# Performance work log

Hardware: AMD Instinct MI355X
Metric: run time of the kernel (lower is better)

The kernel has to match this reference:

```python
import jax, jax.numpy as jnp
import numpy as np

BLOCK_SIZE = 3
SOBEL_PAD = 1  # sobel_size // 2
BLOCK_PAD = BLOCK_SIZE // 2

_SOBEL_X = jnp.array([[-1.0, 0.0, 1.0], [-2.0, 0.0, 2.0], [-1.0, 0.0, 1.0]], dtype=jnp.float32)[None, None]
_SOBEL_Y = jnp.array([[-1.0, -2.0, -1.0], [0.0, 0.0, 0.0], [1.0, 2.0, 1.0]], dtype=jnp.float32)[None, None]
_SUM_K = jnp.ones((1, 1, BLOCK_SIZE, BLOCK_SIZE), dtype=jnp.float32)


def _pad_replicate(x, p):
    return jnp.pad(x, ((0, 0), (0, 0), (p, p), (p, p)), mode='edge')


def _conv(x, k):
    return jax.lax.conv_general_dilated(
        x, k, window_strides=(1, 1), padding='VALID',
        dimension_numbers=('NCHW', 'OIHW', 'NCHW'))


def setup_inputs() -> dict:
    key = jax.random.key(0)
    image = jax.random.uniform(key, (8, 1, 1080, 1920), dtype=jnp.float32) * 255.0
    return {"image": image}


def reference(image) -> jnp.ndarray:
    img = image.astype(jnp.float32)
    img_p = _pad_replicate(img, SOBEL_PAD)
    Ix = _conv(img_p, _SOBEL_X)
    Iy = _conv(img_p, _SOBEL_Y)
    Ixx = Ix * Ix
    Iyy = Iy * Iy
    Ixy = Ix * Iy
    sum_Ixx = _conv(_pad_replicate(Ixx, BLOCK_PAD), _SUM_K)
    sum_Iyy = _conv(_pad_replicate(Iyy, BLOCK_PAD), _SUM_K)
    sum_Ixy = _conv(_pad_replicate(Ixy, BLOCK_PAD), _SUM_K)
    half_trace = (sum_Ixx + sum_Iyy) * 0.5
    diff_half = (sum_Ixx - sum_Iyy) * 0.5
    sqrt_disc = jnp.sqrt(diff_half * diff_half + sum_Ixy * sum_Ixy + 1e-10)
    lambda_min = half_trace - sqrt_disc
    return jnp.clip(lambda_min, 0.0)
```

## Files before the change

### kernel.cpp

```cpp
#include <hip/hip_runtime.h>

typedef float v4f __attribute__((ext_vector_type(4)));

#define IMG_H 1080
#define IMG_W 1920
#define NBATCH 8
#define LSTRIP 9
#define BROWS (4*LSTRIP)
#define NK (LSTRIP+4)
#define PF 3
#define RS 4


__global__ __launch_bounds__(256, 2)
void shi_tomasi_kernel(const float* __restrict__ img, float* __restrict__ out) {
    const int cg    = threadIdx.x & 63;
    const int strip = threadIdx.x >> 6;
    const int bx    = blockIdx.x;
    const int base  = bx * 240;
    const int c0    = base + 4 * (cg - 2);
    const int clA   = min(max(c0 - 2, 0), IMG_W - 4);
    const int clB   = min(max(c0 + 2, 0), IMG_W - 4);
    const int s0    = blockIdx.y * BROWS + strip * LSTRIP;
    const float* g  = img + (size_t)blockIdx.z * (IMG_H * IMG_W);
    float* outb     = out + (size_t)blockIdx.z * (IMG_H * IMG_W);

    const bool eL     = (bx == 0) && (cg == 2);
    const bool eR     = (bx == 7) && (cg == 61);
    const bool doSt   = (cg >= 2) && (cg < 62);
    const bool topFix = (s0 == 0);
    const bool botFix = (s0 + LSTRIP == IMG_H);

    const float* lpA = g + clA;
    const float* lpB = g + clB;

    v4f za[RS], zb[RS];
    #pragma unroll
    for (int k = 0; k < PF; ++k) {
        int lr = max(0, min(IMG_H - 1, s0 - 2 + k));
        za[k] = *(const v4f*)(lpA + (size_t)lr * IMG_W);
        zb[k] = *(const v4f*)(lpB + (size_t)lr * IMG_W);
    }

    float cdR[3][6], hsR[3][6];
    float hxx[3][4], hyy[3][4], hxy[3][4];

    #pragma unroll
    for (int k = 0; k < NK; ++k) {
        if (k + PF < NK) {
            int lr = min(IMG_H - 1, s0 + k + (PF - 2));
            za[(k + PF) % RS] = *(const v4f*)(lpA + (size_t)lr * IMG_W);
            zb[(k + PF) % RS] = *(const v4f*)(lpB + (size_t)lr * IMG_W);
        }

        {
            const v4f A = za[k % RS];
            const v4f B = zb[k % RS];
            const float zm2 = A.x;
            const float zm1 = eL ? A.x : A.y;
            const float z0  = eL ? A.x : A.z;
            const float z1  = eL ? A.y : A.w;
            const float z2  = eR ? B.z : B.x;
            const float z3  = eR ? B.w : B.y;
            const float z4  = eR ? B.w : B.z;
            const float z5  = B.w;

            float* cdw = cdR[k % 3];
            float* hsw = hsR[k % 3];
            cdw[0] = z0 - zm2;
            cdw[1] = z1 - zm1;
            cdw[2] = z2 - z0;
            cdw[3] = z3 - z1;
            cdw[4] = z4 - z2;
            cdw[5] = z5 - z3;
            hsw[0] = fmaf(2.0f, zm1, zm2) + z0;
            hsw[1] = fmaf(2.0f, z0, zm1) + z1;
            hsw[2] = fmaf(2.0f, z1, z0) + z2;
            hsw[3] = fmaf(2.0f, z2, z1) + z3;
            hsw[4] = fmaf(2.0f, z3, z2) + z4;
            hsw[5] = fmaf(2.0f, z4, z3) + z5;
        }

        if (k >= 2) {
            const int rr = k - 2;
            const int sm = rr % 3, sz = (rr + 1) % 3, sp = (rr + 2) % 3;

            float Ix[6], Iy[6];
            #pragma unroll
            for (int p = 0; p < 6; ++p) {
                Ix[p] = fmaf(2.0f, cdR[sz][p], cdR[sm][p]) + cdR[sp][p];
                Iy[p] = hsR[sp][p] - hsR[sm][p];
            }
            if (eL) { Ix[0] = Ix[1]; Iy[0] = Iy[1]; }
            if (eR) { Ix[5] = Ix[4]; Iy[5] = Iy[4]; }

            float xx[6], yy[6], xy[6];
            #pragma unroll
            for (int p = 0; p < 6; ++p) {
                xx[p] = Ix[p] * Ix[p];
                yy[p] = Iy[p] * Iy[p];
                xy[p] = Ix[p] * Iy[p];
            }
            {
                float* hx = hxx[rr % 3];
                float* hy = hyy[rr % 3];
                float* hz = hxy[rr % 3];
                #pragma unroll
                for (int c = 0; c < 4; ++c) {
                    hx[c] = (xx[c] + xx[c + 1]) + xx[c + 2];
                    hy[c] = (yy[c] + yy[c + 1]) + yy[c + 2];
                    hz[c] = (xy[c] + xy[c + 1]) + xy[c + 2];
                }
            }
            if (rr == 1 && topFix) {
                #pragma unroll
                for (int c = 0; c < 4; ++c) {
                    hxx[0][c] = hxx[1][c]; hyy[0][c] = hyy[1][c]; hxy[0][c] = hxy[1][c];
                }
            }
            if (rr == LSTRIP + 1 && botFix) {
                #pragma unroll
                for (int c = 0; c < 4; ++c) {
                    hxx[rr % 3][c] = hxx[(rr - 1) % 3][c];
                    hyy[rr % 3][c] = hyy[(rr - 1) % 3][c];
                    hxy[rr % 3][c] = hxy[(rr - 1) % 3][c];
                }
            }

            if (rr >= 2) {
                const int a = (rr - 2) % 3, b2 = (rr - 1) % 3, cc = rr % 3;
                float rv[4];
                #pragma unroll
                for (int c = 0; c < 4; ++c) {
                    const float sxx = (hxx[a][c] + hxx[b2][c]) + hxx[cc][c];
                    const float syy = (hyy[a][c] + hyy[b2][c]) + hyy[cc][c];
                    const float sxy = (hxy[a][c] + hxy[b2][c]) + hxy[cc][c];
                    const float S = sxx + syy;
                    const float D = sxx - syy;
                    const float E = sxy + sxy;
                    const float disc = fmaf(D, D, fmaf(E, E, 4e-10f));
                    const float q = __builtin_amdgcn_sqrtf(disc);
                    rv[c] = fmaxf((S - q) * 0.5f, 0.0f);
                }
                if (doSt) {
                    float* orowp = outb + (size_t)(s0 + rr - 2) * IMG_W + c0;
                    __builtin_nontemporal_store(v4f{rv[0], rv[1], rv[2], rv[3]},
                                                (v4f*)orowp);
                }
            }
        }
    }
}

extern "C" void kernel_launch(void* const* d_in, const int* in_sizes, int n_in,
                              void* d_out, int out_size, void* d_ws, size_t ws_size,
                              hipStream_t stream) {
    const float* img = (const float*)d_in[0];
    float* out = (float*)d_out;
    dim3 grid(8, IMG_H / BROWS, NBATCH);
    shi_tomasi_kernel<<<grid, 256, 0, stream>>>(img, out);
}
```

Before: 114.1 us.

## Stage block input rows in LDS via global_load_lds instead of per-thread register prefetch

Rather than each thread issuing two overlapping 16-byte global loads per row with a register ring prefetch, the block cooperatively loads 40 halo rows into LDS using direct global-to-LDS loads, then synchronises once. Each thread reads its 8-wide window from LDS with 2-float loads. This removes duplicated global traffic between overlapping column windows and neighbouring strips, at the cost of about 42KB of LDS per block, which may limit occupancy. It also drops the overlap of loads with compute, because the kernel waits on a barrier before any work starts.

```diff
diff --git a/kernel.cpp b/kernel.cpp
--- a/kernel.cpp
+++ b/kernel.cpp
@@ -1,5 +1,6 @@
 #include <hip/hip_runtime.h>
 
+typedef float v2f __attribute__((ext_vector_type(2)));
 typedef float v4f __attribute__((ext_vector_type(4)));
 
 #define IMG_H 1080
@@ -8,20 +9,21 @@
 #define LSTRIP 9
 #define BROWS (4*LSTRIP)
 #define NK (LSTRIP+4)
-#define PF 3
-#define RS 4
+#define NROWS 40
+#define ROWF 264
 
 
 __global__ __launch_bounds__(256, 2)
 void shi_tomasi_kernel(const float* __restrict__ img, float* __restrict__ out) {
+    __shared__ float lds[NROWS * ROWF];
+
     const int cg    = threadIdx.x & 63;
     const int strip = threadIdx.x >> 6;
     const int bx    = blockIdx.x;
     const int base  = bx * 240;
     const int c0    = base + 4 * (cg - 2);
-    const int clA   = min(max(c0 - 2, 0), IMG_W - 4);
-    const int clB   = min(max(c0 + 2, 0), IMG_W - 4);
-    const int s0    = blockIdx.y * BROWS + strip * LSTRIP;
+    const int S0    = blockIdx.y * BROWS;
+    const int s0    = S0 + strip * LSTRIP;
     const float* g  = img + (size_t)blockIdx.z * (IMG_H * IMG_W);
     float* outb     = out + (size_t)blockIdx.z * (IMG_H * IMG_W);
 
@@ -31,39 +33,40 @@
     const bool topFix = (s0 == 0);
     const bool botFix = (s0 + LSTRIP == IMG_H);
 
-    const float* lpA = g + clA;
-    const float* lpB = g + clB;
+    const int cl = min(max(base - 8 + 4 * cg, 0), IMG_W - 4);
 
-    v4f za[RS], zb[RS];
     #pragma unroll
-    for (int k = 0; k < PF; ++k) {
-        int lr = max(0, min(IMG_H - 1, s0 - 2 + k));
-        za[k] = *(const v4f*)(lpA + (size_t)lr * IMG_W);
-        zb[k] = *(const v4f*)(lpB + (size_t)lr * IMG_W);
+    for (int t = 0; t < 10; ++t) {
+        const int j = strip * 10 + t;
+        const int r = min(max(S0 - 2 + j, 0), IMG_H - 1);
+        __builtin_amdgcn_global_load_lds(
+            (const __attribute__((address_space(1))) void*)(g + (size_t)r * IMG_W + cl),
+            (__attribute__((address_space(3))) void*)&lds[j * ROWF],
+            16, 0, 0);
     }
+    __syncthreads();
 
     float cdR[3][6], hsR[3][6];
     float hxx[3][4], hyy[3][4], hxy[3][4];
 
+    const int qoff = max(4 * cg - 2, 0);
+
     #pragma unroll
     for (int k = 0; k < NK; ++k) {
-        if (k + PF < NK) {
-            int lr = min(IMG_H - 1, s0 + k + (PF - 2));
-            za[(k + PF) % RS] = *(const v4f*)(lpA + (size_t)lr * IMG_W);
-            zb[(k + PF) % RS] = *(const v4f*)(lpB + (size_t)lr * IMG_W);
-        }
-
         {
-            const v4f A = za[k % RS];
-            const v4f B = zb[k % RS];
-            const float zm2 = A.x;
-            const float zm1 = eL ? A.x : A.y;
-            const float z0  = eL ? A.x : A.z;
-            const float z1  = eL ? A.y : A.w;
-            const float z2  = eR ? B.z : B.x;
-            const float z3  = eR ? B.w : B.y;
-            const float z4  = eR ? B.w : B.z;
-            const float z5  = B.w;
+            const float* lr = &lds[(9 * strip + k) * ROWF + qoff];
+            const v2f D0 = *(const v2f*)(lr);
+            const v2f D1 = *(const v2f*)(lr + 2);
+            const v2f D2 = *(const v2f*)(lr + 4);
+            const v2f D3 = *(const v2f*)(lr + 6);
+            const float zm2 = eL ? D1.x : D0.x;
+            const float zm1 = eL ? D1.x : D0.y;
+            const float z0  = D1.x;
+            const float z1  = D1.y;
+            const float z2  = D2.x;
+            const float z3  = D2.y;
+            const float z4  = eR ? D2.y : D3.x;
+            const float z5  = eR ? D2.y : D3.y;
 
             float* cdw = cdR[k % 3];
             float* hsw = hsR[k % 3];
```

New measurement: 113.0 us. No clear change (-0.9%).
